# Kernel optimization log

Measured on AMD Instinct MI355X. Metric: run time of the kernel, lower is better.

Reference implementation:

```python
import jax, jax.numpy as jnp
import numpy as np

D_MODEL = 1024
NUM_HEADS = 16
D_K = D_MODEL // NUM_HEADS
THETA = 10000.0


def _apply_rope(x, positions):
    # x: [B, H, S, d_k], positions: [B, S]
    dk = x.shape[-1]
    freq = 1.0 / (THETA ** (jnp.arange(0, dk, 2, dtype=jnp.float32) / dk))  # [dk/2]
    ang = positions.astype(jnp.float32)[:, None, :, None] * freq  # [B,1,S,dk/2]
    cos, sin = jnp.cos(ang), jnp.sin(ang)
    x_even = x[..., 0::2]
    x_odd = x[..., 1::2]
    re = x_even * cos - x_odd * sin
    ro = x_even * sin + x_odd * cos
    # interleave back: [..., dk/2, 2] -> [..., dk]
    return jnp.stack([re, ro], axis=-1).reshape(x.shape)


def setup_inputs() -> dict:
    key = jax.random.key(0)
    kx, kq, kk, kv, ko = jax.random.split(key, 5)
    B, S = 2, 2048
    std = (2.0 / (D_MODEL + D_MODEL)) ** 0.5
    x = jax.random.normal(kx, (B, S, D_MODEL), dtype=jnp.float32)
    Wq = jax.random.normal(kq, (D_MODEL, D_MODEL), dtype=jnp.float32) * std
    Wk = jax.random.normal(kk, (D_MODEL, D_MODEL), dtype=jnp.float32) * std
    Wv = jax.random.normal(kv, (D_MODEL, D_MODEL), dtype=jnp.float32) * std
    Wo = jax.random.normal(ko, (D_MODEL, D_MODEL), dtype=jnp.float32) * std
    token_positions = jnp.tile(jnp.arange(S, dtype=jnp.int32)[None, :], (B, 1))
    return {"x": x, "Wq": Wq, "Wk": Wk, "Wv": Wv, "Wo": Wo,
            "token_positions": token_positions}


def reference(x, Wq, Wk, Wv, Wo, token_positions):
    B, S, D = x.shape
    H, dk = NUM_HEADS, D_K
    scale = 1.0 / np.sqrt(dk)
    # Linear is y = x @ W.T with W:[d_out, d_in]
    q = jnp.einsum('bsd,ed->bse', x, Wq).reshape(B, S, H, dk).transpose(0, 2, 1, 3)
    k = jnp.einsum('bsd,ed->bse', x, Wk).reshape(B, S, H, dk).transpose(0, 2, 1, 3)
    v = jnp.einsum('bsd,ed->bse', x, Wv).reshape(B, S, H, dk).transpose(0, 2, 1, 3)
    q = _apply_rope(q, token_positions)
    k = _apply_rope(k, token_positions)
    scores = jnp.einsum('bhqd,bhkd->bhqk', q, k) * scale  # [B,H,S,S]
    causal = jnp.tril(jnp.ones((S, S), dtype=bool))
    scores = jnp.where(causal[None, None, :, :], scores, -jnp.inf)
    probs = jax.nn.softmax(scores, axis=-1)
    attn = jnp.einsum('bhqk,bhkd->bhqd', probs, v)  # [B,H,S,dk]
    attn = attn.transpose(0, 2, 1, 3).reshape(B, S, D)
    return jnp.einsum('bsd,ed->bse', attn, Wo)
```

## Files before the change

### kernel.cpp

```cpp
#include <hip/hip_runtime.h>
#include <hip/hip_bf16.h>
#include <math.h>

#define B_  2
#define S_  2048
#define H_  16
#define D_  1024
#define DK_ 64

typedef __attribute__((ext_vector_type(8))) short bf16x8;
typedef __attribute__((ext_vector_type(8))) unsigned short ushort8v;
typedef __attribute__((ext_vector_type(4))) float f32x4;

__device__ __forceinline__ unsigned short f2bf(float f) {
  unsigned u = __float_as_uint(f);
  unsigned r = (u + 0x7FFFu + ((u >> 16) & 1u)) >> 16;
  return (unsigned short)r;
}
__device__ __forceinline__ unsigned pack_trunc(float lo, float hi) {
  return (__float_as_uint(lo) >> 16) | (__float_as_uint(hi) & 0xffff0000u);
}
__device__ __forceinline__ float fast_exp2(float x) {
#if __has_builtin(__builtin_amdgcn_exp2f)
  return __builtin_amdgcn_exp2f(x);
#else
  return __expf(x * 0.69314718056f);
#endif
}
__device__ __forceinline__ void gload_lds16(const unsigned short* g,
                                            unsigned short* l) {
  __builtin_amdgcn_global_load_lds(
      (const __attribute__((address_space(1))) unsigned int*)(const void*)g,
      (__attribute__((address_space(3))) unsigned int*)(void*)l, 16, 0, 0);
}

__global__ __launch_bounds__(256)
void cast5_bf16(const float* __restrict__ x,  const float* __restrict__ wq,
                const float* __restrict__ wk, const float* __restrict__ wv,
                const float* __restrict__ wo,
                unsigned short* __restrict__ xb,  unsigned short* __restrict__ wqb,
                unsigned short* __restrict__ wkb, unsigned short* __restrict__ wvb,
                unsigned short* __restrict__ wob)
{
  const int idx = blockIdx.x;
  const float* s; unsigned short* d; int lblk;
  if (idx < 2048) { s = x; d = xb; lblk = idx; }
  else {
    int t = idx - 2048;
    int w = t >> 9;
    lblk  = t & 511;
    s = (w == 0) ? wq  : (w == 1) ? wk  : (w == 2) ? wv  : wo;
    d = (w == 0) ? wqb : (w == 1) ? wkb : (w == 2) ? wvb : wob;
  }
  size_t i0 = ((size_t)lblk * 256 + threadIdx.x) * 8;
  float4 v0 = *(const float4*)(s + i0);
  float4 v1 = *(const float4*)(s + i0 + 4);
  ushort8v o;
  o[0] = f2bf(v0.x); o[1] = f2bf(v0.y); o[2] = f2bf(v0.z); o[3] = f2bf(v0.w);
  o[4] = f2bf(v1.x); o[5] = f2bf(v1.y); o[6] = f2bf(v1.z); o[7] = f2bf(v1.w);
  *(ushort8v*)(d + i0) = o;
}

__global__ __launch_bounds__(256)
void gemm_qkv(const unsigned short* __restrict__ A0,
              const unsigned short* __restrict__ W0,
              const unsigned short* __restrict__ W1,
              const unsigned short* __restrict__ W2,
              unsigned short* __restrict__ qh,
              unsigned short* __restrict__ kh,
              unsigned short* __restrict__ vt,
              const int* __restrict__ tp)
{
  const int z = blockIdx.z;

  const int f  = blockIdx.x + (blockIdx.y << 3);
  const int bx = (f >> 3) & 7;
  const int by = (f & 7) | ((f >> 6) << 3);

  __shared__ unsigned short As[128 * 64];
  __shared__ unsigned short Bs[128 * 64];
  __shared__ int tps[128];

  const int tid   = threadIdx.x;
  const int wave  = tid >> 6;
  const int lane  = tid & 63;
  const int quad  = lane >> 4;
  const int col16 = lane & 15;
  const int wr    = (wave >> 1) * 64;
  const int wc    = (wave & 1) * 64;

  const int row0 = (z == 2) ? bx * 128 : by * 128;
  const int col0 = (z == 2) ? by * 128 : bx * 128;
  const unsigned short* Aptr = (z == 2) ? W2 : A0;
  const unsigned short* Bptr = (z == 0) ? W0 : (z == 1) ? W1 : A0;

  if (z < 2 && tid < 128) tps[tid] = tp[row0 + tid];

  const int srow = wave * 8 + (lane >> 3);
  const int scol = ((lane & 7) ^ ((lane >> 3) & 7)) * 8;
  const unsigned short* gA = Aptr + (size_t)(row0 + srow) * D_ + scol;
  const unsigned short* gB = Bptr + (size_t)(col0 + srow) * D_ + scol;

  f32x4 acc[4][4];
  #pragma unroll
  for (int mt = 0; mt < 4; ++mt)
    #pragma unroll
    for (int nt = 0; nt < 4; ++nt)
      #pragma unroll
      for (int r = 0; r < 4; ++r) acc[mt][nt][r] = 0.f;

  for (int k0 = 0; k0 < D_; k0 += 64) {
    __syncthreads();
    #pragma unroll
    for (int p = 0; p < 4; ++p) {
      gload_lds16(gA + (size_t)(p * 32) * D_ + k0, &As[(p * 32 + wave * 8) * 64]);
      gload_lds16(gB + (size_t)(p * 32) * D_ + k0, &Bs[(p * 32 + wave * 8) * 64]);
    }
    __syncthreads();

    #pragma unroll
    for (int h = 0; h < 2; ++h) {
      const int jo = ((h * 4 + quad) ^ (col16 & 7)) * 8;
      bf16x8 af[4], bfr[4];
      #pragma unroll
      for (int mt = 0; mt < 4; ++mt)
        af[mt] = *(const bf16x8*)&As[(wr + mt * 16 + col16) * 64 + jo];
      #pragma unroll
      for (int nt = 0; nt < 4; ++nt)
        bfr[nt] = *(const bf16x8*)&Bs[(wc + nt * 16 + col16) * 64 + jo];

      #pragma unroll
      for (int mt = 0; mt < 4; ++mt)
        #pragma unroll
        for (int nt = 0; nt < 4; ++nt)
          acc[mt][nt] = __builtin_amdgcn_mfma_f32_16x16x32_bf16(
              af[mt], bfr[nt], acc[mt][nt], 0, 0, 0);
    }
  }

  if (z == 2) {
    #pragma unroll
    for (int mt = 0; mt < 4; ++mt)
      #pragma unroll
      for (int r = 0; r < 4; ++r) {
        int c = row0 + wr + mt * 16 + quad * 4 + r;
        int h = c >> 6, d = c & 63;
        #pragma unroll
        for (int nt = 0; nt < 4; ++nt) {
          int t  = col0 + wc + nt * 16 + col16;
          int bb = t >> 11, sl = t & (S_ - 1);
          vt[((size_t)((bb << 4) + h) * DK_ + d) * S_ + sl] =
              f2bf(acc[mt][nt][r]);
        }
      }
  } else {
    unsigned short* C = z ? kh : qh;
    const float qs = z ? 1.0f : 0.1803368801111204f;
    const float sgn = (col16 & 1) ? 1.f : -1.f;
    float freqr[4];
    #pragma unroll
    for (int nt = 0; nt < 4; ++nt) {
      int i = ((wc + nt * 16 + col16) & 63) >> 1;
      freqr[nt] = exp2f(-0.4152410118f * (float)i);
    }
    #pragma unroll
    for (int mt = 0; mt < 4; ++mt)
      #pragma unroll
      for (int r = 0; r < 4; ++r) {
        int rl  = wr + mt * 16 + quad * 4 + r;
        int row = row0 + rl;
        float p = (float)tps[rl];
        #pragma unroll
        for (int nt = 0; nt < 4; ++nt) {
          int col = col0 + wc + nt * 16 + col16;
          float ang = p * freqr[nt];
          float sn = __sinf(ang), cs = __cosf(ang);
          float val = acc[mt][nt][r];
          float oth = __shfl_xor(val, 1);
          C[(size_t)row * D_ + col] = f2bf((val * cs + oth * sgn * sn) * qs);
        }
      }
  }
}

__global__ __launch_bounds__(256)
void gemm_wo(const unsigned short* __restrict__ A,
             const unsigned short* __restrict__ W,
             float* __restrict__ C)
{
  __shared__ unsigned short As[64 * 64];
  __shared__ unsigned short Bs[128 * 64];

  const int f  = blockIdx.x + (blockIdx.y << 3);
  const int bx = (f >> 3) & 7;
  const int by = (f & 7) | ((f >> 6) << 3);

  const int tid   = threadIdx.x;
  const int wave  = tid >> 6;
  const int lane  = tid & 63;
  const int quad  = lane >> 4;
  const int col16 = lane & 15;
  const int row0  = by * 64;
  const int col0  = bx * 128;
  const int wr    = (wave >> 1) * 32;
  const int wc    = (wave & 1) * 64;

  const int srow = wave * 8 + (lane >> 3);
  const int scol = ((lane & 7) ^ ((lane >> 3) & 7)) * 8;
  const unsigned short* gA = A + (size_t)(row0 + srow) * D_ + scol;
  const unsigned short* gB = W + (size_t)(col0 + srow) * D_ + scol;

  f32x4 acc[2][4];
  #pragma unroll
  for (int mt = 0; mt < 2; ++mt)
    #pragma unroll
    for (int nt = 0; nt < 4; ++nt)
      #pragma unroll
      for (int r = 0; r < 4; ++r) acc[mt][nt][r] = 0.f;

  for (int k0 = 0; k0 < D_; k0 += 64) {
    __syncthreads();
    #pragma unroll
    for (int p = 0; p < 2; ++p)
      gload_lds16(gA + (size_t)(p * 32) * D_ + k0, &As[(p * 32 + wave * 8) * 64]);
    #pragma unroll
    for (int p = 0; p < 4; ++p)
      gload_lds16(gB + (size_t)(p * 32) * D_ + k0, &Bs[(p * 32 + wave * 8) * 64]);
    __syncthreads();

    #pragma unroll
    for (int h = 0; h < 2; ++h) {
      const int jo = ((h * 4 + quad) ^ (col16 & 7)) * 8;
      bf16x8 af[2], bfr[4];
      #pragma unroll
      for (int mt = 0; mt < 2; ++mt)
        af[mt] = *(const bf16x8*)&As[(wr + mt * 16 + col16) * 64 + jo];
      #pragma unroll
      for (int nt = 0; nt < 4; ++nt)
        bfr[nt] = *(const bf16x8*)&Bs[(wc + nt * 16 + col16) * 64 + jo];

      #pragma unroll
      for (int mt = 0; mt < 2; ++mt)
        #pragma unroll
        for (int nt = 0; nt < 4; ++nt)
          acc[mt][nt] = __builtin_amdgcn_mfma_f32_16x16x32_bf16(
              af[mt], bfr[nt], acc[mt][nt], 0, 0, 0);
    }
  }

  #pragma unroll
  for (int mt = 0; mt < 2; ++mt)
    #pragma unroll
    for (int r = 0; r < 4; ++r) {
      int row = row0 + wr + mt * 16 + quad * 4 + r;
      #pragma unroll
      for (int nt = 0; nt < 4; ++nt) {
        int col = col0 + wc + nt * 16 + col16;
        C[(size_t)row * D_ + col] = acc[mt][nt][r];
      }
    }
}

__global__ __launch_bounds__(512, 6)
void attn_mfma(const unsigned short* __restrict__ Q,
               const unsigned short* __restrict__ K,
               const unsigned short* __restrict__ Vt,
               unsigned short* __restrict__ O)
{
  const int f   = blockIdx.x;
  const int qt  = 31 - (f >> 5);
  const int bh  = f & 31;
  const int b   = bh >> 4, h = bh & 15;

  const int tid  = threadIdx.x;
  const int w    = tid >> 6;
  const int lane = tid & 63;
  const int quad = lane >> 4;
  const int col  = lane & 15;
  const int rw   = w & 3;
  const int p    = w >> 2;
  const int qlocal = rw * 16 + col;

  __shared__ unsigned short Ks[2 * 4096];
  __shared__ unsigned short Vs[2 * 4096];
  __shared__ __align__(16) unsigned short Pl[8][16][72];

  const size_t qkbase = (size_t)b * S_ * D_ + (size_t)h * DK_;
  const size_t vtbase = (size_t)bh * DK_ * S_;

  const int qrow = qt * 64 + qlocal;
  bf16x8 qf[2];
  qf[0] = *(const bf16x8*)(Q + qkbase + (size_t)qrow * D_ + quad * 8);
  qf[1] = *(const bf16x8*)(Q + qkbase + (size_t)qrow * D_ + 32 + quad * 8);

  const int lr8 = lane >> 3;
  const int sj  = ((lane & 7) ^ (lr8 & 7)) * 8;

  auto stageK = [&](int g) {
    const int gc = (g > qt) ? qt : g;
    const unsigned short* s =
        K + qkbase + (size_t)(gc * 64 + rw * 16 + lr8) * D_ + sj;
    #pragma unroll
    for (int pp = 0; pp < 2; ++pp)
      gload_lds16(s + (size_t)(pp * 8) * D_, &Ks[p * 4096 + (rw * 16 + pp * 8) * 64]);
  };
  auto stageV = [&](int g) {
    const int gc = (g > qt) ? qt : g;
    const unsigned short* s =
        Vt + vtbase + (size_t)(rw * 16 + lr8) * S_ + gc * 64 + sj;
    #pragma unroll
    for (int pp = 0; pp < 2; ++pp)
      gload_lds16(s + (size_t)(pp * 8) * S_, &Vs[p * 4096 + (rw * 16 + pp * 8) * 64]);
  };

  f32x4 Oacc[4];
  #pragma unroll
  for (int nb = 0; nb < 4; ++nb)
    #pragma unroll
    for (int r = 0; r < 4; ++r) Oacc[nb][r] = 0.f;
  float l_i = 0.f;

  const int M  = (qt >> 1) + 1;
  const int jx = quad ^ (col & 7);
  const unsigned short* KsH = Ks + p * 4096;
  const unsigned short* VsH = Vs + p * 4096;
  unsigned short (*Plw)[72] = Pl[w];

  stageK(p);
  stageV(p);
  asm volatile("s_waitcnt vmcnt(0)" ::: "memory");
  __builtin_amdgcn_s_barrier();
  __builtin_amdgcn_sched_barrier(0);

  for (int m = 0; m < M; ++m) {
    const int g    = 2 * m + p;
    const bool act = (g <= qt);
    const bool dg  = (g == qt);

    f32x4 st[4];
    if (act) {
      __builtin_amdgcn_s_setprio(1);
      #pragma unroll
      for (int nb = 0; nb < 4; ++nb) {
        const int s0 = (nb * 16 + col) * 8 + jx;
        bf16x8 ka0 = *(const bf16x8*)(KsH + s0 * 8);
        bf16x8 ka1 = *(const bf16x8*)(KsH + (s0 ^ 4) * 8);
        f32x4 a = {-24.f, -24.f, -24.f, -24.f};
        a = __builtin_amdgcn_mfma_f32_16x16x32_bf16(ka0, qf[0], a, 0, 0, 0);
        a = __builtin_amdgcn_mfma_f32_16x16x32_bf16(ka1, qf[1], a, 0, 0, 0);
        st[nb] = a;
      }
      __builtin_amdgcn_s_setprio(0);
    }
    __builtin_amdgcn_sched_barrier(0);
    __builtin_amdgcn_s_barrier();
    __builtin_amdgcn_sched_barrier(0);

    stageK(2 * m + 2 + p);

    if (act) {
      if (dg) {
        #pragma unroll
        for (int nb = 0; nb < 4; ++nb)
          #pragma unroll
          for (int r = 0; r < 4; ++r)
            if (nb * 16 + quad * 4 + r > qlocal) st[nb][r] = -1e30f;
      }
      float rsum = 0.f;
      #pragma unroll
      for (int nb = 0; nb < 4; ++nb)
        #pragma unroll
        for (int r = 0; r < 4; ++r) {
          float pv = fast_exp2(st[nb][r]);
          st[nb][r] = pv;
          rsum += pv;
        }
      rsum += __shfl_xor(rsum, 16);
      rsum += __shfl_xor(rsum, 32);
      l_i += rsum;
      #pragma unroll
      for (int nb = 0; nb < 4; ++nb) {
        uint2 pk;
        pk.x = pack_trunc(st[nb][0], st[nb][1]);
        pk.y = pack_trunc(st[nb][2], st[nb][3]);
        *(uint2*)&Plw[col][nb * 16 + quad * 4] = pk;
      }
    }

    asm volatile("s_waitcnt vmcnt(2)" ::: "memory");
    __builtin_amdgcn_sched_barrier(0);
    __builtin_amdgcn_s_barrier();
    __builtin_amdgcn_sched_barrier(0);

    if (act) {
      bf16x8 pf0 = *(const bf16x8*)&Plw[col][quad * 8];
      bf16x8 pf1 = *(const bf16x8*)&Plw[col][32 + quad * 8];
      __builtin_amdgcn_s_setprio(1);
      #pragma unroll
      for (int nb = 0; nb < 4; ++nb) {
        const int s0 = (nb * 16 + col) * 8 + jx;
        bf16x8 va0 = *(const bf16x8*)(VsH + s0 * 8);
        bf16x8 va1 = *(const bf16x8*)(VsH + (s0 ^ 4) * 8);
        Oacc[nb] = __builtin_amdgcn_mfma_f32_16x16x32_bf16(va0, pf0, Oacc[nb], 0, 0, 0);
        Oacc[nb] = __builtin_amdgcn_mfma_f32_16x16x32_bf16(va1, pf1, Oacc[nb], 0, 0, 0);
      }
      __builtin_amdgcn_s_setprio(0);
    }
    __builtin_amdgcn_sched_barrier(0);
    __builtin_amdgcn_s_barrier();
    __builtin_amdgcn_sched_barrier(0);

    stageV(2 * m + 2 + p);
    asm volatile("s_waitcnt vmcnt(2)" ::: "memory");
    __builtin_amdgcn_sched_barrier(0);
    __builtin_amdgcn_s_barrier();
    __builtin_amdgcn_sched_barrier(0);
  }

  asm volatile("s_waitcnt vmcnt(0)" ::: "memory");
  __syncthreads();
  float* sc = (float*)&Pl[0][0][0];
  if (p == 1) {
    float* d0 = sc + ((size_t)(rw * 64 + lane)) * 18;
    #pragma unroll
    for (int nb = 0; nb < 4; ++nb)
      #pragma unroll
      for (int r = 0; r < 4; ++r) d0[nb * 4 + r] = Oacc[nb][r];
    d0[16] = l_i;
  }
  __syncthreads();
  if (p == 0) {
    const float* s0 = sc + ((size_t)(rw * 64 + lane)) * 18;
    const float inv = 1.0f / (l_i + s0[16]);
    #pragma unroll
    for (int nb = 0; nb < 4; ++nb) {
      int d = nb * 16 + quad * 4;
      ushort4 oa;
      oa.x = f2bf((Oacc[nb][0] + s0[nb * 4 + 0]) * inv);
      oa.y = f2bf((Oacc[nb][1] + s0[nb * 4 + 1]) * inv);
      oa.z = f2bf((Oacc[nb][2] + s0[nb * 4 + 2]) * inv);
      oa.w = f2bf((Oacc[nb][3] + s0[nb * 4 + 3]) * inv);
      *(ushort4*)(O + (size_t)b * S_ * D_ + (size_t)qrow * D_ + h * DK_ + d) = oa;
    }
  }
}

extern "C" void kernel_launch(void* const* d_in, const int* in_sizes, int n_in,
                              void* d_out, int out_size, void* d_ws, size_t ws_size,
                              hipStream_t stream)
{
  const float* x  = (const float*)d_in[0];
  const float* Wq = (const float*)d_in[1];
  const float* Wk = (const float*)d_in[2];
  const float* Wv = (const float*)d_in[3];
  const float* Wo = (const float*)d_in[4];
  const int*   tp = (const int*)d_in[5];
  float* out = (float*)d_out;

  const size_t NTOK = (size_t)B_ * S_ * D_;
  const size_t NW   = (size_t)D_ * D_;
  unsigned short* qh  = (unsigned short*)d_ws;
  unsigned short* kh  = qh + NTOK;
  unsigned short* vt  = kh + NTOK;
  unsigned short* xb  = vt + NTOK;
  unsigned short* wqb = xb + NTOK;
  unsigned short* wkb = wqb + NW;
  unsigned short* wvb = wkb + NW;
  unsigned short* wob = wvb + NW;
  unsigned short* ab  = xb;

  cast5_bf16<<<dim3(4096), 256, 0, stream>>>(
      x, Wq, Wk, Wv, Wo, xb, wqb, wkb, wvb, wob);

  gemm_qkv<<<dim3(D_ / 128, (B_ * S_) / 128, 3), 256, 0, stream>>>(
      xb, wqb, wkb, wvb, qh, kh, vt, tp);

  attn_mfma<<<dim3(32 * 32), 512, 0, stream>>>(qh, kh, vt, ab);

  gemm_wo<<<dim3(D_ / 128, (B_ * S_) / 64), 256, 0, stream>>>(ab, wob, out);
}
```

Before: 171.4 us.

## Double-buffer LDS tiles in QKV and output projection GEMMs

Both projection GEMMs now use two LDS buffers and issue the global-to-LDS loads for the next K tile before computing on the current one. Partial vmcnt waits and raw s_barriers with sched_barrier fences replace the two __syncthreads per iteration. The aim is to hide global load latency behind MFMA work. The cost is doubled LDS use, which may lower occupancy, and hand-counted vmcnt values that must match the number of loads issued per stage.

```diff
diff --git a/kernel.cpp b/kernel.cpp
--- a/kernel.cpp
+++ b/kernel.cpp
@@ -77,8 +77,8 @@
   const int bx = (f >> 3) & 7;
   const int by = (f & 7) | ((f >> 6) << 3);
 
-  __shared__ unsigned short As[128 * 64];
-  __shared__ unsigned short Bs[128 * 64];
+  __shared__ unsigned short As[2][128 * 64];
+  __shared__ unsigned short Bs[2][128 * 64];
   __shared__ int tps[128];
 
   const int tid   = threadIdx.x;
@@ -109,25 +109,41 @@
       #pragma unroll
       for (int r = 0; r < 4; ++r) acc[mt][nt][r] = 0.f;
 
-  for (int k0 = 0; k0 < D_; k0 += 64) {
-    __syncthreads();
+  auto stage = [&](int k) {
+    const int k0 = k << 6;
+    unsigned short* Ad = &As[k & 1][wave * 8 * 64];
+    unsigned short* Bd = &Bs[k & 1][wave * 8 * 64];
     #pragma unroll
     for (int p = 0; p < 4; ++p) {
-      gload_lds16(gA + (size_t)(p * 32) * D_ + k0, &As[(p * 32 + wave * 8) * 64]);
-      gload_lds16(gB + (size_t)(p * 32) * D_ + k0, &Bs[(p * 32 + wave * 8) * 64]);
-    }
-    __syncthreads();
-
+      gload_lds16(gA + (size_t)(p * 32) * D_ + k0, Ad + (p * 32) * 64);
+      gload_lds16(gB + (size_t)(p * 32) * D_ + k0, Bd + (p * 32) * 64);
+    }
+  };
+
+  stage(0);
+  for (int k = 0; k < 16; ++k) {
+    if (k < 15) {
+      stage(k + 1);
+      asm volatile("s_waitcnt vmcnt(8)" ::: "memory");
+    } else {
+      asm volatile("s_waitcnt vmcnt(0)" ::: "memory");
+    }
+    __builtin_amdgcn_sched_barrier(0);
+    __builtin_amdgcn_s_barrier();
+    __builtin_amdgcn_sched_barrier(0);
+
+    const unsigned short* Ac = &As[k & 1][0];
+    const unsigned short* Bc = &Bs[k & 1][0];
     #pragma unroll
     for (int h = 0; h < 2; ++h) {
       const int jo = ((h * 4 + quad) ^ (col16 & 7)) * 8;
       bf16x8 af[4], bfr[4];
       #pragma unroll
       for (int mt = 0; mt < 4; ++mt)
-        af[mt] = *(const bf16x8*)&As[(wr + mt * 16 + col16) * 64 + jo];
+        af[mt] = *(const bf16x8*)&Ac[(wr + mt * 16 + col16) * 64 + jo];
       #pragma unroll
       for (int nt = 0; nt < 4; ++nt)
-        bfr[nt] = *(const bf16x8*)&Bs[(wc + nt * 16 + col16) * 64 + jo];
+        bfr[nt] = *(const bf16x8*)&Bc[(wc + nt * 16 + col16) * 64 + jo];
 
       #pragma unroll
       for (int mt = 0; mt < 4; ++mt)
@@ -135,6 +151,12 @@
         for (int nt = 0; nt < 4; ++nt)
           acc[mt][nt] = __builtin_amdgcn_mfma_f32_16x16x32_bf16(
               af[mt], bfr[nt], acc[mt][nt], 0, 0, 0);
+    }
+
+    if (k < 15) {
+      __builtin_amdgcn_sched_barrier(0);
+      __builtin_amdgcn_s_barrier();
+      __builtin_amdgcn_sched_barrier(0);
     }
   }
 
@@ -188,8 +210,8 @@
              const unsigned short* __restrict__ W,
              float* __restrict__ C)
 {
-  __shared__ unsigned short As[64 * 64];
-  __shared__ unsigned short Bs[128 * 64];
+  __shared__ unsigned short As[2][64 * 64];
+  __shared__ unsigned short Bs[2][128 * 64];
 
   const int f  = blockIdx.x + (blockIdx.y << 3);
   const int bx = (f >> 3) & 7;
@@ -218,26 +240,42 @@
       #pragma unroll
       for (int r = 0; r < 4; ++r) acc[mt][nt][r] = 0.f;
 
-  for (int k0 = 0; k0 < D_; k0 += 64) {
-    __syncthreads();
+  auto stage = [&](int k) {
+    const int k0 = k << 6;
+    unsigned short* Ad = &As[k & 1][wave * 8 * 64];
+    unsigned short* Bd = &Bs[k & 1][wave * 8 * 64];
     #pragma unroll
     for (int p = 0; p < 2; ++p)
-      gload_lds16(gA + (size_t)(p * 32) * D_ + k0, &As[(p * 32 + wave * 8) * 64]);
+      gload_lds16(gA + (size_t)(p * 32) * D_ + k0, Ad + (p * 32) * 64);
     #pragma unroll
     for (int p = 0; p < 4; ++p)
-      gload_lds16(gB + (size_t)(p * 32) * D_ + k0, &Bs[(p * 32 + wave * 8) * 64]);
-    __syncthreads();
-
+      gload_lds16(gB + (size_t)(p * 32) * D_ + k0, Bd + (p * 32) * 64);
+  };
+
+  stage(0);
+  for (int k = 0; k < 16; ++k) {
+    if (k < 15) {
+      stage(k + 1);
+      asm volatile("s_waitcnt vmcnt(6)" ::: "memory");
+    } else {
+      asm volatile("s_waitcnt vmcnt(0)" ::: "memory");
+    }
+    __builtin_amdgcn_sched_barrier(0);
+    __builtin_amdgcn_s_barrier();
+    __builtin_amdgcn_sched_barrier(0);
+
+    const unsigned short* Ac = &As[k & 1][0];
+    const unsigned short* Bc = &Bs[k & 1][0];
     #pragma unroll
     for (int h = 0; h < 2; ++h) {
       const int jo = ((h * 4 + quad) ^ (col16 & 7)) * 8;
       bf16x8 af[2], bfr[4];
       #pragma unroll
       for (int mt = 0; mt < 2; ++mt)
-        af[mt] = *(const bf16x8*)&As[(wr + mt * 16 + col16) * 64 + jo];
+        af[mt] = *(const bf16x8*)&Ac[(wr + mt * 16 + col16) * 64 + jo];
       #pragma unroll
       for (int nt = 0; nt < 4; ++nt)
-        bfr[nt] = *(const bf16x8*)&Bs[(wc + nt * 16 + col16) * 64 + jo];
+        bfr[nt] = *(const bf16x8*)&Bc[(wc + nt * 16 + col16) * 64 + jo];
 
       #pragma unroll
       for (int mt = 0; mt < 2; ++mt)
@@ -245,6 +283,12 @@
         for (int nt = 0; nt < 4; ++nt)
           acc[mt][nt] = __builtin_amdgcn_mfma_f32_16x16x32_bf16(
               af[mt], bfr[nt], acc[mt][nt], 0, 0, 0);
+    }
+
+    if (k < 15) {
+      __builtin_amdgcn_sched_barrier(0);
+      __builtin_amdgcn_s_barrier();
+      __builtin_amdgcn_sched_barrier(0);
     }
   }
 
```

Measured after the change: 172.4 us. No clear change (+0.5%).
